# Kernel optimization log

Hardware: AMD Instinct MI355X
Metric: run time of the kernel (lower is better)

## Reference

```python
import jax, jax.numpy as jnp
import numpy as np

B, C, H, W = 64, 256, 64, 64
HEADS = 8
Q = 16
FH = 512
EPS = 1e-6


def setup_inputs() -> dict:
    key = jax.random.key(0)
    ks = jax.random.split(key, 4)
    def init(k, shape, fan_in):
        return jax.random.normal(k, shape, jnp.float32) * (1.0 / np.sqrt(fan_in))
    return {
        "x": jax.random.normal(ks[0], (B, C, H, W), jnp.float32),
        "ln_gamma": jnp.ones((C,), jnp.float32),
        "ln_beta": jnp.zeros((C,), jnp.float32),
        # grouped 1x1 conv weight: torch shape [Q*h, C/h, 1, 1] -> [h, Q, C/h]
        "attn_w": init(ks[1], (HEADS, Q, C // HEADS), C // HEADS),
        "val_w": init(ks[2], (C, C), C),
        "val_b": jnp.zeros((C,), jnp.float32),
        "fin_w": init(ks[3], (FH, C * Q), C * Q),
        "fin_b": jnp.zeros((FH,), jnp.float32),
    }


def reference(x, ln_gamma, ln_beta, attn_w, val_w, val_b, fin_w, fin_b):
    B_, C_, H_, W_ = x.shape
    L = H_ * W_
    xf = x.reshape(B_, C_, L)  # [B, C, HW]
    # LayerNorm2d: normalize over channel dim (permute in torch == axis=1 here)
    mu = jnp.mean(xf, axis=1, keepdims=True)
    var = jnp.mean((xf - mu) ** 2, axis=1, keepdims=True)
    xn = (xf - mu) * jax.lax.rsqrt(var + EPS) * ln_gamma[:, None] + ln_beta[:, None]
    # grouped 1x1 conv: each head sees its own C/h channel slice
    xh = xn.reshape(B_, HEADS, C_ // HEADS, L)
    logits = jnp.einsum('hqc,bhcl->bhql', attn_w, xh)  # [B, h, Q, HW]
    Aw = jax.nn.softmax(logits, axis=-1)
    # value projection: full 1x1 conv with bias
    V = jnp.einsum('ec,bcl->bel', val_w, xn) + val_b[None, :, None]  # [B, C, HW]
    Vh = V.reshape(B_, HEADS, C_ // HEADS, L)
    # weighted pooling (bmm): [B, h, Q, d]
    A = jnp.einsum('bhql,bhdl->bhqd', Aw, Vh)
    Aflat = A.reshape(B_, Q * C_)  # matches torch reshape order (h, q, d)
    return Aflat @ fin_w.T + fin_b
```

## Files before the change

### kernel.cpp

```cpp
#include <hip/hip_runtime.h>

typedef unsigned short u16;
typedef unsigned int u32;

#define B_   64
#define C_   256
#define L_   4096
#define NH   8
#define NQ   16
#define DH   32
#define HQ   128
#define FHN  512
#define EPS_ 1e-6f

#define WS_XBF   0
#define WS_MU    134217728
#define WS_RS    135266304
#define WS_DEN   136314880
#define WS_SNUM  136347648
#define WS_WC    136380416
#define WS_SWG   136388608
#define WS_CB    136389120
#define WS_A     136389632
#define WS_PP    137438208

typedef __attribute__((ext_vector_type(8))) short bf16x8;
typedef __attribute__((ext_vector_type(4))) float f32x4;

__device__ __forceinline__ u16 f32_to_bf16(float f) {
    u32 u = __float_as_uint(f);
    u32 r = u + 0x7fffu + ((u >> 16) & 1u);
    return (u16)(r >> 16);
}
__device__ __forceinline__ float bf16_to_f32(u16 h) {
    return __uint_as_float(((u32)h) << 16);
}
__device__ __forceinline__ u32 pk2(u16 lo, u16 hi) {
    return (u32)lo | ((u32)hi << 16);
}

__global__ __launch_bounds__(256) void k_prep(
    const float* __restrict__ attn_w, const float* __restrict__ gamma,
    const float* __restrict__ beta, u16* __restrict__ wc,
    float* __restrict__ Swg, float* __restrict__ Cb)
{
    int t = threadIdx.x;
    if (t >= HQ) return;
    int h = t >> 4;
    float sw = 0.f, cb = 0.f;
    for (int c = 0; c < DH; c++) {
        float w = attn_w[t * DH + c];
        u16 hb = f32_to_bf16(w * gamma[h * DH + c]);
        wc[t * DH + c] = hb;
        sw += bf16_to_f32(hb);
        cb += w * beta[h * DH + c];
    }
    Swg[t] = sw;
    Cb[t] = cb;
}

__global__ __launch_bounds__(256) void k_stats(
    const float* __restrict__ x, u16* __restrict__ xbf,
    float* __restrict__ mu, float* __restrict__ rs)
{
    int g = blockIdx.x * 256 + threadIdx.x;
    int b = g >> 11;
    int l = (g & 2047) * 2;
    const float* xb = x + (size_t)b * C_ * L_ + l;
    u16* xo = xbf + (size_t)b * C_ * L_ + l;
    float s0 = 0, s1 = 0, q0 = 0, q1 = 0;
    for (int c = 0; c < C_; c++) {
        float2 v = *(const float2*)(xb + (size_t)c * L_);
        s0 += v.x; q0 += v.x * v.x;
        s1 += v.y; q1 += v.y * v.y;
        *(u32*)(xo + (size_t)c * L_) = pk2(f32_to_bf16(v.x), f32_to_bf16(v.y));
    }
    float2 m, r;
    float mm, vv;
    mm = s0 * (1.f / C_); vv = fmaxf(q0 * (1.f / C_) - mm * mm, 0.f) + EPS_;
    m.x = mm; r.x = rsqrtf(vv);
    mm = s1 * (1.f / C_); vv = fmaxf(q1 * (1.f / C_) - mm * mm, 0.f) + EPS_;
    m.y = mm; r.y = rsqrtf(vv);
    size_t o = (size_t)b * L_ + l;
    *(float2*)(mu + o) = m;
    *(float2*)(rs + o) = r;
}

__global__ __launch_bounds__(256) void k_fused(
    const u16* __restrict__ xbf, const u16* __restrict__ wc,
    const float* __restrict__ Swg, const float* __restrict__ Cb,
    const float* __restrict__ mu, const float* __restrict__ rs,
    float* __restrict__ Pp, float* __restrict__ denom, float* __restrict__ Snum)
{
    __shared__ u16 XT[32 * 264];
    __shared__ u16 EA[128 * 40];
    __shared__ u16 XC[2][256 * 32];
    int t = threadIdx.x;
    int lane = t & 63, wv = t >> 6;
    int lane15 = lane & 15, quad = lane >> 4;
    int ks = blockIdx.x, b = blockIdx.y;
    int lbase = ks * 512;
    int m0 = (wv & 1) * 64, n0 = (wv >> 1) * 128;

    bf16x8 af[2];
    float swr[2][4], cbr[2][4];
    #pragma unroll
    for (int s = 0; s < 2; s++) {
        int h = wv * 2 + s;
        af[s] = *(const bf16x8*)(wc + (size_t)(h * 16 + lane15) * DH + quad * 8);
        #pragma unroll
        for (int r = 0; r < 4; r++) {
            int hq = h * 16 + quad * 4 + r;
            swr[s][r] = Swg[hq];
            cbr[s][r] = Cb[hq];
        }
    }

    const u16* xbR = xbf + ((size_t)b * C_ + t) * L_ + lbase;
    const float* mub = mu + (size_t)b * L_ + lbase;
    const float* rsb = rs + (size_t)b * L_ + lbase;

    uint4 xr[4];
    auto loadregs = [&](int k) {
        int o = k * 32;
        #pragma unroll
        for (int i = 0; i < 4; i++) xr[i] = *(const uint4*)(xbR + o + i * 8);
    };
    auto write_xc = [&](int buf) {
        #pragma unroll
        for (int i = 0; i < 4; i++)
            *(uint4*)&XC[buf][t * 32 + ((i ^ (t & 3)) * 8)] = xr[i];
    };
    auto write_xt = [&]() {
        const u16* ph = (const u16*)xr;
        #pragma unroll
        for (int e = 0; e < 32; e++) XT[e * 264 + t] = ph[e];
    };

    f32x4 acc[4][8];
    #pragma unroll
    for (int i = 0; i < 4; i++)
        #pragma unroll
        for (int j = 0; j < 8; j++) {
            f32x4 z = {0.f, 0.f, 0.f, 0.f};
            acc[i][j] = z;
        }
    float se[2][4] = {}, sm[2][4] = {};
    float muc[2], rsc[2], mun[2] = {}, rsn[2] = {};
    muc[0] = mub[lane15]; muc[1] = mub[16 + lane15];
    rsc[0] = rsb[lane15]; rsc[1] = rsb[16 + lane15];

    loadregs(0);
    write_xc(0);
    write_xt();
    loadregs(1);
    __syncthreads();

    for (int k = 0; k < 16; k++) {
        int cur = k & 1;
        if (k < 15) {
            mun[0] = mub[(k + 1) * 32 + lane15]; mun[1] = mub[(k + 1) * 32 + 16 + lane15];
            rsn[0] = rsb[(k + 1) * 32 + lane15]; rsn[1] = rsb[(k + 1) * 32 + 16 + lane15];
        }
        #pragma unroll
        for (int s = 0; s < 2; s++) {
            int h = wv * 2 + s;
            #pragma unroll
            for (int half = 0; half < 2; half++) {
                bf16x8 bfrag = *(const bf16x8*)(XT + (half * 16 + lane15) * 264 + h * DH + quad * 8);
                f32x4 z = {0.f, 0.f, 0.f, 0.f};
                f32x4 c4 = __builtin_amdgcn_mfma_f32_16x16x32_bf16(af[s], bfrag, z, 0, 0, 0);
                float m_l = muc[half], r_l = rsc[half];
                #pragma unroll
                for (int r = 0; r < 4; r++) {
                    float logit = r_l * (c4[r] - m_l * swr[s][r]) + cbr[s][r];
                    float e = __expf(logit);
                    float ers = e * r_l;
                    EA[(h * 16 + quad * 4 + r) * 40 + half * 16 + lane15] = f32_to_bf16(ers);
                    se[s][r] += e;
                    sm[s][r] += ers * m_l;
                }
            }
        }
        __syncthreads();

        if (k < 15) { write_xc(cur ^ 1); write_xt(); }
        if (k < 14) loadregs(k + 2);

        bf16x8 a[4];
        #pragma unroll
        for (int i = 0; i < 4; i++)
            a[i] = *(const bf16x8*)&EA[(m0 + i * 16 + lane15) * 40 + quad * 8];
        #pragma unroll
        for (int j = 0; j < 8; j++) {
            int row = n0 + j * 16 + lane15;
            bf16x8 bbj = *(const bf16x8*)&XC[cur][row * 32 + ((quad ^ (row & 3)) * 8)];
            #pragma unroll
            for (int i = 0; i < 4; i++)
                acc[i][j] = __builtin_amdgcn_mfma_f32_16x16x32_bf16(a[i], bbj, acc[i][j], 0, 0, 0);
        }
        __syncthreads();

        muc[0] = mun[0]; muc[1] = mun[1];
        rsc[0] = rsn[0]; rsc[1] = rsn[1];
    }

    float* PpB = Pp + (((size_t)ks * B_ + b) * HQ) * C_;
    #pragma unroll
    for (int i = 0; i < 4; i++)
        #pragma unroll
        for (int r = 0; r < 4; r++) {
            int hq = m0 + i * 16 + quad * 4 + r;
            #pragma unroll
            for (int j = 0; j < 8; j++)
                PpB[(size_t)hq * C_ + n0 + j * 16 + lane15] = acc[i][j][r];
        }

    #pragma unroll
    for (int s = 0; s < 2; s++)
        #pragma unroll
        for (int r = 0; r < 4; r++) {
            float v = se[s][r], w = sm[s][r];
            #pragma unroll
            for (int off = 1; off < 16; off <<= 1) {
                v += __shfl_xor(v, off);
                w += __shfl_xor(w, off);
            }
            if (lane15 == 0) {
                int row = b * HQ + (wv * 2 + s) * 16 + quad * 4 + r;
                atomicAdd(&denom[row], v);
                atomicAdd(&Snum[row], w);
            }
        }
}

__global__ __launch_bounds__(256) void k_attn_pool(
    const float* __restrict__ Pp, const float* __restrict__ denom,
    const float* __restrict__ Snum, const float* __restrict__ gamma,
    const float* __restrict__ beta, const float* __restrict__ val_w,
    const float* __restrict__ val_b, float* __restrict__ A)
{
    __shared__ float Pt[NQ * 257];
    __shared__ float Vw[DH * 257];
    __shared__ float vb_s[DH];
    int t = threadIdx.x;
    int h = blockIdx.x, b = blockIdx.y;

    for (int i = t; i < DH * C_; i += 256) {
        int r = i >> 8, c = i & 255;
        Vw[r * 257 + c] = val_w[(h * DH + r) * C_ + c];
    }
    if (t < DH) vb_s[t] = val_b[h * DH + t];

    const float* PpB = Pp + ((size_t)b * HQ + h * NQ) * C_;
    const size_t sstr = (size_t)B_ * HQ * C_;
    for (int i = t; i < NQ * C_; i += 256) {
        int q = i >> 8, c = i & 255;
        int hq = h * NQ + q;
        float d = denom[b * HQ + hq];
        float sn = Snum[b * HQ + hq];
        float pv = 0.f;
        #pragma unroll
        for (int s = 0; s < 8; s++) pv += PpB[s * sstr + (size_t)q * C_ + c];
        Pt[q * 257 + c] = gamma[c] * (pv - sn) / d + beta[c];
    }
    __syncthreads();

    int q = t >> 4, dd = (t & 15) * 2;
    float a0 = vb_s[dd], a1 = vb_s[dd + 1];
    for (int c = 0; c < C_; c++) {
        float pv = Pt[q * 257 + c];
        a0 += pv * Vw[dd * 257 + c];
        a1 += pv * Vw[(dd + 1) * 257 + c];
    }
    size_t off = ((size_t)(b * HQ + h * NQ + q)) * DH + dd;
    A[off] = a0; A[off + 1] = a1;
}

__global__ __launch_bounds__(256) void k_final(
    const float* __restrict__ A, const float* __restrict__ fin_w,
    const float* __restrict__ fin_b, float* __restrict__ out)
{
    __shared__ float At[64 * 129];
    __shared__ float Fw[32 * 129];
    int t = threadIdx.x;
    int kc = blockIdx.x, ft = blockIdx.y;
    int k0 = kc * 128;

    #pragma unroll
    for (int w = 0; w < 8; w++) {
        int s = t + w * 256;
        int row = s >> 5, seg = s & 31;
        float4 v = *(const float4*)(A + (size_t)row * 4096 + k0 + seg * 4);
        const float* pf = (const float*)&v;
        #pragma unroll
        for (int e = 0; e < 4; e++) At[row * 129 + seg * 4 + e] = pf[e];
    }
    #pragma unroll
    for (int w = 0; w < 4; w++) {
        int s = t + w * 256;
        int row = s >> 5, seg = s & 31;
        float4 v = *(const float4*)(fin_w + (size_t)(ft * 32 + row) * 4096 + k0 + seg * 4);
        const float* pf = (const float*)&v;
        #pragma unroll
        for (int e = 0; e < 4; e++) Fw[row * 129 + seg * 4 + e] = pf[e];
    }
    __syncthreads();

    int tb = t >> 3, tf = t & 7;
    float acc[2][4];
    #pragma unroll
    for (int e = 0; e < 2; e++)
        #pragma unroll
        for (int j = 0; j < 4; j++) acc[e][j] = 0.f;

    for (int k = 0; k < 128; k++) {
        float a0 = At[(tb * 2) * 129 + k];
        float a1 = At[(tb * 2 + 1) * 129 + k];
        #pragma unroll
        for (int j = 0; j < 4; j++) {
            float f = Fw[(tf * 4 + j) * 129 + k];
            acc[0][j] += a0 * f;
            acc[1][j] += a1 * f;
        }
    }
    #pragma unroll
    for (int e = 0; e < 2; e++) {
        int brow = tb * 2 + e;
        #pragma unroll
        for (int j = 0; j < 4; j++) {
            int f = ft * 32 + tf * 4 + j;
            float v = acc[e][j];
            if (kc == 0) v += fin_b[f];
            atomicAdd(&out[(size_t)brow * FHN + f], v);
        }
    }
}

extern "C" void kernel_launch(void* const* d_in, const int* in_sizes, int n_in,
                              void* d_out, int out_size, void* d_ws, size_t ws_size,
                              hipStream_t stream) {
    const float* x      = (const float*)d_in[0];
    const float* gamma  = (const float*)d_in[1];
    const float* beta   = (const float*)d_in[2];
    const float* attn_w = (const float*)d_in[3];
    const float* val_w  = (const float*)d_in[4];
    const float* val_b  = (const float*)d_in[5];
    const float* fin_w  = (const float*)d_in[6];
    const float* fin_b  = (const float*)d_in[7];
    float* out = (float*)d_out;
    char* ws = (char*)d_ws;

    u16*   xbf   = (u16*)(ws + WS_XBF);
    float* mu    = (float*)(ws + WS_MU);
    float* rs    = (float*)(ws + WS_RS);
    float* denom = (float*)(ws + WS_DEN);
    float* Snum  = (float*)(ws + WS_SNUM);
    u16*   wc    = (u16*)(ws + WS_WC);
    float* Swg   = (float*)(ws + WS_SWG);
    float* Cb    = (float*)(ws + WS_CB);
    float* A     = (float*)(ws + WS_A);
    float* Pp    = (float*)(ws + WS_PP);

    hipMemsetAsync(denom, 0, 65536, stream);
    hipMemsetAsync(out, 0, (size_t)B_ * FHN * sizeof(float), stream);

    k_prep<<<dim3(1), dim3(256), 0, stream>>>(attn_w, gamma, beta, wc, Swg, Cb);
    k_stats<<<dim3(512), dim3(256), 0, stream>>>(x, xbf, mu, rs);
    k_fused<<<dim3(8, 64), dim3(256), 0, stream>>>(xbf, wc, Swg, Cb, mu, rs,
                                                   Pp, denom, Snum);
    k_attn_pool<<<dim3(8, 64), dim3(256), 0, stream>>>(Pp, denom, Snum, gamma,
                                                       beta, val_w, val_b, A);
    k_final<<<dim3(32, 16), dim3(256), 0, stream>>>(A, fin_w, fin_b, out);
}
```

Before: 500.8 us.

## Fuse LayerNorm statistics and bf16 conversion into the main fused kernel

Removes the separate stats kernel that read fp32 x and wrote a bf16 copy plus mean/rstd. The fused kernel now loads fp32 x directly, converts to bf16 in registers, and computes per-position channel statistics from the LDS tile each iteration. This cuts global memory traffic substantially. Atomic accumulation of denominators is replaced by per-split partial buffers summed in the pool kernel, which drops a memset. In exchange it adds register pressure from doubled fp32 loads, an extra barrier per iteration, and computes statistics from bf16-rounded values.

```diff
diff --git a/kernel.cpp b/kernel.cpp
--- a/kernel.cpp
+++ b/kernel.cpp
@@ -13,16 +13,13 @@
 #define FHN  512
 #define EPS_ 1e-6f
 
-#define WS_XBF   0
-#define WS_MU    134217728
-#define WS_RS    135266304
-#define WS_DEN   136314880
-#define WS_SNUM  136347648
-#define WS_WC    136380416
-#define WS_SWG   136388608
-#define WS_CB    136389120
-#define WS_A     136389632
-#define WS_PP    137438208
+#define WS_WC    0
+#define WS_SWG   8192
+#define WS_CB    8704
+#define WS_DENP  9216
+#define WS_SNUP  271360
+#define WS_A     533504
+#define WS_PP    1582080
 
 typedef __attribute__((ext_vector_type(8))) short bf16x8;
 typedef __attribute__((ext_vector_type(4))) float f32x4;
@@ -59,42 +56,15 @@
     Cb[t] = cb;
 }
 
-__global__ __launch_bounds__(256) void k_stats(
-    const float* __restrict__ x, u16* __restrict__ xbf,
-    float* __restrict__ mu, float* __restrict__ rs)
-{
-    int g = blockIdx.x * 256 + threadIdx.x;
-    int b = g >> 11;
-    int l = (g & 2047) * 2;
-    const float* xb = x + (size_t)b * C_ * L_ + l;
-    u16* xo = xbf + (size_t)b * C_ * L_ + l;
-    float s0 = 0, s1 = 0, q0 = 0, q1 = 0;
-    for (int c = 0; c < C_; c++) {
-        float2 v = *(const float2*)(xb + (size_t)c * L_);
-        s0 += v.x; q0 += v.x * v.x;
-        s1 += v.y; q1 += v.y * v.y;
-        *(u32*)(xo + (size_t)c * L_) = pk2(f32_to_bf16(v.x), f32_to_bf16(v.y));
-    }
-    float2 m, r;
-    float mm, vv;
-    mm = s0 * (1.f / C_); vv = fmaxf(q0 * (1.f / C_) - mm * mm, 0.f) + EPS_;
-    m.x = mm; r.x = rsqrtf(vv);
-    mm = s1 * (1.f / C_); vv = fmaxf(q1 * (1.f / C_) - mm * mm, 0.f) + EPS_;
-    m.y = mm; r.y = rsqrtf(vv);
-    size_t o = (size_t)b * L_ + l;
-    *(float2*)(mu + o) = m;
-    *(float2*)(rs + o) = r;
-}
-
 __global__ __launch_bounds__(256) void k_fused(
-    const u16* __restrict__ xbf, const u16* __restrict__ wc,
+    const float* __restrict__ x, const u16* __restrict__ wc,
     const float* __restrict__ Swg, const float* __restrict__ Cb,
-    const float* __restrict__ mu, const float* __restrict__ rs,
-    float* __restrict__ Pp, float* __restrict__ denom, float* __restrict__ Snum)
+    float* __restrict__ Pp, float* __restrict__ DenP, float* __restrict__ SnuP)
 {
     __shared__ u16 XT[32 * 264];
     __shared__ u16 EA[128 * 40];
     __shared__ u16 XC[2][256 * 32];
+    __shared__ float smu[32], srs[32];
     int t = threadIdx.x;
     int lane = t & 63, wv = t >> 6;
     int lane15 = lane & 15, quad = lane >> 4;
@@ -116,23 +86,37 @@
         }
     }
 
-    const u16* xbR = xbf + ((size_t)b * C_ + t) * L_ + lbase;
-    const float* mub = mu + (size_t)b * L_ + lbase;
-    const float* rsb = rs + (size_t)b * L_ + lbase;
-
-    uint4 xr[4];
+    const float* xR = x + ((size_t)b * C_ + t) * L_ + lbase;
+
+    float4 fr[8];
+    uint4 pr[4];
     auto loadregs = [&](int k) {
         int o = k * 32;
         #pragma unroll
-        for (int i = 0; i < 4; i++) xr[i] = *(const uint4*)(xbR + o + i * 8);
+        for (int i = 0; i < 8; i++) fr[i] = *(const float4*)(xR + o + i * 4);
+    };
+    auto cvtregs = [&]() {
+        const float* pf = (const float*)fr;
+        u16 hh[32];
+        #pragma unroll
+        for (int e = 0; e < 32; e++) hh[e] = f32_to_bf16(pf[e]);
+        #pragma unroll
+        for (int i = 0; i < 4; i++) {
+            uint4 w;
+            w.x = pk2(hh[i * 8 + 0], hh[i * 8 + 1]);
+            w.y = pk2(hh[i * 8 + 2], hh[i * 8 + 3]);
+            w.z = pk2(hh[i * 8 + 4], hh[i * 8 + 5]);
+            w.w = pk2(hh[i * 8 + 6], hh[i * 8 + 7]);
+            pr[i] = w;
+        }
     };
     auto write_xc = [&](int buf) {
         #pragma unroll
         for (int i = 0; i < 4; i++)
-            *(uint4*)&XC[buf][t * 32 + ((i ^ (t & 3)) * 8)] = xr[i];
+            *(uint4*)&XC[buf][t * 32 + ((i ^ (t & 3)) * 8)] = pr[i];
     };
     auto write_xt = [&]() {
-        const u16* ph = (const u16*)xr;
+        const u16* ph = (const u16*)pr;
         #pragma unroll
         for (int e = 0; e < 32; e++) XT[e * 264 + t] = ph[e];
     };
@@ -146,31 +130,58 @@
             acc[i][j] = z;
         }
     float se[2][4] = {}, sm[2][4] = {};
-    float muc[2], rsc[2], mun[2] = {}, rsn[2] = {};
-    muc[0] = mub[lane15]; muc[1] = mub[16 + lane15];
-    rsc[0] = rsb[lane15]; rsc[1] = rsb[16 + lane15];
+
+    int l_loc = t >> 3, g = t & 7;
 
     loadregs(0);
+    cvtregs();
+    write_xt();
     write_xc(0);
-    write_xt();
     loadregs(1);
     __syncthreads();
 
     for (int k = 0; k < 16; k++) {
         int cur = k & 1;
-        if (k < 15) {
-            mun[0] = mub[(k + 1) * 32 + lane15]; mun[1] = mub[(k + 1) * 32 + 16 + lane15];
-            rsn[0] = rsb[(k + 1) * 32 + lane15]; rsn[1] = rsb[(k + 1) * 32 + 16 + lane15];
-        }
-        #pragma unroll
-        for (int s = 0; s < 2; s++) {
-            int h = wv * 2 + s;
-            #pragma unroll
-            for (int half = 0; half < 2; half++) {
+
+        {
+            const u16* row = XT + l_loc * 264 + g * 32;
+            float s = 0.f, q = 0.f;
+            #pragma unroll
+            for (int j = 0; j < 4; j++) {
+                uint4 v = *(const uint4*)(row + j * 8);
+                u32 ww[4] = {v.x, v.y, v.z, v.w};
+                #pragma unroll
+                for (int e = 0; e < 4; e++) {
+                    float f0 = __uint_as_float(ww[e] << 16);
+                    float f1 = __uint_as_float(ww[e] & 0xffff0000u);
+                    s += f0 + f1;
+                    q += f0 * f0 + f1 * f1;
+                }
+            }
+            #pragma unroll
+            for (int off = 1; off < 8; off <<= 1) {
+                s += __shfl_xor(s, off);
+                q += __shfl_xor(q, off);
+            }
+            if (g == 0) {
+                float mm = s * (1.f / C_);
+                float vv = fmaxf(q * (1.f / C_) - mm * mm, 0.f) + EPS_;
+                smu[l_loc] = mm;
+                srs[l_loc] = rsqrtf(vv);
+            }
+        }
+        __syncthreads();
+
+        #pragma unroll
+        for (int half = 0; half < 2; half++) {
+            float m_l = smu[half * 16 + lane15];
+            float r_l = srs[half * 16 + lane15];
+            #pragma unroll
+            for (int s = 0; s < 2; s++) {
+                int h = wv * 2 + s;
                 bf16x8 bfrag = *(const bf16x8*)(XT + (half * 16 + lane15) * 264 + h * DH + quad * 8);
                 f32x4 z = {0.f, 0.f, 0.f, 0.f};
                 f32x4 c4 = __builtin_amdgcn_mfma_f32_16x16x32_bf16(af[s], bfrag, z, 0, 0, 0);
-                float m_l = muc[half], r_l = rsc[half];
                 #pragma unroll
                 for (int r = 0; r < 4; r++) {
                     float logit = r_l * (c4[r] - m_l * swr[s][r]) + cbr[s][r];
@@ -184,7 +195,7 @@
         }
         __syncthreads();
 
-        if (k < 15) { write_xc(cur ^ 1); write_xt(); }
+        if (k < 15) { cvtregs(); write_xt(); write_xc(cur ^ 1); }
         if (k < 14) loadregs(k + 2);
 
         bf16x8 a[4];
@@ -200,9 +211,6 @@
                 acc[i][j] = __builtin_amdgcn_mfma_f32_16x16x32_bf16(a[i], bbj, acc[i][j], 0, 0, 0);
         }
         __syncthreads();
-
-        muc[0] = mun[0]; muc[1] = mun[1];
-        rsc[0] = rsn[0]; rsc[1] = rsn[1];
     }
 
     float* PpB = Pp + (((size_t)ks * B_ + b) * HQ) * C_;
@@ -228,15 +236,15 @@
             }
             if (lane15 == 0) {
                 int row = b * HQ + (wv * 2 + s) * 16 + quad * 4 + r;
-                atomicAdd(&denom[row], v);
-                atomicAdd(&Snum[row], w);
+                DenP[ks * (B_ * HQ) + row] = v;
+                SnuP[ks * (B_ * HQ) + row] = w;
             }
         }
 }
 
 __global__ __launch_bounds__(256) void k_attn_pool(
-    const float* __restrict__ Pp, const float* __restrict__ denom,
-    const float* __restrict__ Snum, const float* __restrict__ gamma,
+    const float* __restrict__ Pp, const float* __restrict__ DenP,
+    const float* __restrict__ SnuP, const float* __restrict__ gamma,
     const float* __restrict__ beta, const float* __restrict__ val_w,
     const float* __restrict__ val_b, float* __restrict__ A)
 {
@@ -256,9 +264,13 @@
     const size_t sstr = (size_t)B_ * HQ * C_;
     for (int i = t; i < NQ * C_; i += 256) {
         int q = i >> 8, c = i & 255;
-        int hq = h * NQ + q;
-        float d = denom[b * HQ + hq];
-        float sn = Snum[b * HQ + hq];
+        int row = b * HQ + h * NQ + q;
+        float d = 0.f, sn = 0.f;
+        #pragma unroll
+        for (int s = 0; s < 8; s++) {
+            d += DenP[s * (B_ * HQ) + row];
+            sn += SnuP[s * (B_ * HQ) + row];
+        }
         float pv = 0.f;
         #pragma unroll
         for (int s = 0; s < 8; s++) pv += PpB[s * sstr + (size_t)q * C_ + c];
@@ -351,25 +363,19 @@
     float* out = (float*)d_out;
     char* ws = (char*)d_ws;
 
-    u16*   xbf   = (u16*)(ws + WS_XBF);
-    float* mu    = (float*)(ws + WS_MU);
-    float* rs    = (float*)(ws + WS_RS);
-    float* denom = (float*)(ws + WS_DEN);
-    float* Snum  = (float*)(ws + WS_SNUM);
     u16*   wc    = (u16*)(ws + WS_WC);
     float* Swg   = (float*)(ws + WS_SWG);
     float* Cb    = (float*)(ws + WS_CB);
+    float* DenP  = (float*)(ws + WS_DENP);
+    float* SnuP  = (float*)(ws + WS_SNUP);
     float* A     = (float*)(ws + WS_A);
     float* Pp    = (float*)(ws + WS_PP);
 
-    hipMemsetAsync(denom, 0, 65536, stream);
     hipMemsetAsync(out, 0, (size_t)B_ * FHN * sizeof(float), stream);
 
     k_prep<<<dim3(1), dim3(256), 0, stream>>>(attn_w, gamma, beta, wc, Swg, Cb);
-    k_stats<<<dim3(512), dim3(256), 0, stream>>>(x, xbf, mu, rs);
-    k_fused<<<dim3(8, 64), dim3(256), 0, stream>>>(xbf, wc, Swg, Cb, mu, rs,
-                                                   Pp, denom, Snum);
-    k_attn_pool<<<dim3(8, 64), dim3(256), 0, stream>>>(Pp, denom, Snum, gamma,
+    k_fused<<<dim3(8, 64), dim3(256), 0, stream>>>(x, wc, Swg, Cb, Pp, DenP, SnuP);
+    k_attn_pool<<<dim3(8, 64), dim3(256), 0, stream>>>(Pp, DenP, SnuP, gamma,
                                                        beta, val_w, val_b, A);
     k_final<<<dim3(32, 16), dim3(256), 0, stream>>>(A, fin_w, fin_b, out);
 }
```

After: 442.4 us. 11.7% less time.
